# Kernel tuning notes

Hardware: AMD Instinct MI355X
Metric: run time of the kernel (lower is better)

The kernel has to match this reference:

```python
import jax, jax.numpy as jnp
import numpy as np

SOFTCAP = 50.0  # GEMMA2_TANH_SCALE
N_HEADS = 16

def _rope(x, cos, sin):
    # x: [B,S,H,D]; cos/sin: [S,D/2]; interleaved complex pairs as in apply_rotary_emb
    x0 = x[..., 0::2]
    x1 = x[..., 1::2]
    c = cos[None, :, None, :]
    s = sin[None, :, None, :]
    r0 = x0 * c - x1 * s
    r1 = x0 * s + x1 * c
    return jnp.stack([r0, r1], axis=-1).reshape(x.shape)

def setup_inputs() -> dict:
    key = jax.random.key(0)
    ks = jax.random.split(key, 5)
    B, S, DM = 1, 2048, 2048
    hd = DM // N_HEADS
    scale = 1.0 / np.sqrt(DM)
    x = jax.random.normal(ks[0], (B, S, DM), jnp.float32)
    wq = jax.random.normal(ks[1], (DM, DM), jnp.float32) * scale
    wk = jax.random.normal(ks[2], (DM, DM), jnp.float32) * scale
    wv = jax.random.normal(ks[3], (DM, DM), jnp.float32) * scale
    wo = jax.random.normal(ks[4], (DM, DM), jnp.float32) * scale
    # rotary tables, theta=10000 as in llama
    inv_freq = 10000.0 ** (-jnp.arange(0, hd, 2, dtype=jnp.float32) / hd)
    ang = jnp.arange(S, dtype=jnp.float32)[:, None] * inv_freq[None, :]
    return {"x": x, "wq": wq, "wk": wk, "wv": wv, "wo": wo,
            "freqs_cos": jnp.cos(ang), "freqs_sin": jnp.sin(ang)}

def reference(x, wq, wk, wv, wo, freqs_cos, freqs_sin):
    B, S, DM = x.shape
    H = N_HEADS
    hd = DM // H
    q = (x @ wq).reshape(B, S, H, hd)
    k = (x @ wk).reshape(B, S, H, hd)
    v = (x @ wv).reshape(B, S, H, hd)
    q = _rope(q, freqs_cos, freqs_sin)
    k = _rope(k, freqs_cos, freqs_sin)
    # scores [B,H,S,S]
    scores = jnp.einsum('bqhd,bkhd->bhqk', q, k) / jnp.sqrt(jnp.float32(hd))
    scores = SOFTCAP * jnp.tanh(scores / SOFTCAP)  # gemma2 tanh soft-cap
    causal = jnp.tril(jnp.ones((S, S), dtype=bool))
    scores = jnp.where(causal[None, None], scores, -jnp.inf)
    p = jax.nn.softmax(scores, axis=-1)
    o = jnp.einsum('bhqk,bkhd->bqhd', p, v).reshape(B, S, DM)
    return o @ wo
```

## Files before the change

### kernel.cpp

```cpp
#include <hip/hip_runtime.h>
#include <hip/hip_bf16.h>

typedef __attribute__((ext_vector_type(8))) short short8;
typedef __attribute__((ext_vector_type(4))) short short4v;
typedef __attribute__((ext_vector_type(4))) float f32x4;
typedef __attribute__((ext_vector_type(4))) float float4v;

#define S_LEN 2048
#define DMODEL 2048
#define N_HEADS 16
#define HEAD_DIM 128
#define NKT 32

__device__ __forceinline__ float bf2f(__hip_bfloat16 b) { return __bfloat162float(b); }
__device__ __forceinline__ __hip_bfloat16 f2bf(float f) { return __float2bfloat16(f); }
__device__ __forceinline__ short bfs(float f) {
    union { __hip_bfloat16 b; short s; } x; x.b = __float2bfloat16(f); return x.s;
}
__device__ __forceinline__ float sbf(short s) {
    union { short s; __hip_bfloat16 b; } x; x.s = s; return __bfloat162float(x.b);
}

#if __has_builtin(__builtin_amdgcn_global_load_lds)
#define HAVE_ASYNC_LDS 1
#else
#define HAVE_ASYNC_LDS 0
#endif

__device__ __forceinline__ void stage16(const __hip_bfloat16* g, __hip_bfloat16* ldsbase, int lane) {
#if HAVE_ASYNC_LDS
    __builtin_amdgcn_global_load_lds(
        (const __attribute__((address_space(1))) unsigned int*)g,
        (__attribute__((address_space(3))) unsigned int*)ldsbase,
        16, 0, 0);
#else
    *(short8*)((char*)ldsbase + lane * 16) = *(const short8*)g;
#endif
}

__global__ __launch_bounds__(256) void prep(const float* __restrict__ x,
                                            const float* __restrict__ w0,
                                            const float* __restrict__ w1,
                                            const float* __restrict__ w2,
                                            const float* __restrict__ w3,
                                            __hip_bfloat16* __restrict__ xb,
                                            __hip_bfloat16* __restrict__ o0,
                                            __hip_bfloat16* __restrict__ o1,
                                            __hip_bfloat16* __restrict__ o2,
                                            __hip_bfloat16* __restrict__ o3) {
    const int z = blockIdx.z;
    const int tid = threadIdx.x;
    if (z == 4) {
        size_t base = (((size_t)blockIdx.y * 32 + blockIdx.x) * 256 + tid) * 16;
        for (int i = 0; i < 4; ++i) {
            float4v v = *(const float4v*)(x + base + i * 4);
            short4v p;
            p.x = bfs(v.x); p.y = bfs(v.y); p.z = bfs(v.z); p.w = bfs(v.w);
            *(short4v*)((short*)xb + base + i * 4) = p;
        }
        return;
    }
    const float* in = (z == 0) ? w0 : (z == 1) ? w1 : (z == 2) ? w2 : w3;
    __hip_bfloat16* out = (z == 0) ? o0 : (z == 1) ? o1 : (z == 2) ? o2 : o3;
    __shared__ short tile[64][68];
    const int bx = blockIdx.x * 64;
    const int by = blockIdx.y * 64;
    const int c4 = (tid & 15) * 4;
    for (int rr = 0; rr < 4; ++rr) {
        int r = (tid >> 4) + rr * 16;
        float4v v = *(const float4v*)(in + (size_t)(by + r) * DMODEL + bx + c4);
        short4v p;
        p.x = bfs(v.x); p.y = bfs(v.y); p.z = bfs(v.z); p.w = bfs(v.w);
        *(short4v*)&tile[r][c4] = p;
    }
    __syncthreads();
    const int oc = tid >> 2;
    const int s0 = (tid & 3) * 16;
    short8 a, b;
    for (int i = 0; i < 8; ++i) ((short*)&a)[i] = tile[s0 + i][oc];
    for (int i = 0; i < 8; ++i) ((short*)&b)[i] = tile[s0 + 8 + i][oc];
    *(short8*)((short*)out + (size_t)(bx + oc) * DMODEL + by + s0) = a;
    *(short8*)((short*)out + (size_t)(bx + oc) * DMODEL + by + s0 + 8) = b;
}


#define CFENCE asm volatile("" ::: "memory")
#define BARRIER do { CFENCE; __builtin_amdgcn_s_barrier(); CFENCE; } while (0)
#define WAIT_LGKM0 asm volatile("s_waitcnt lgkmcnt(0)" ::: "memory")
#define WAIT_VM(n) asm volatile("s_waitcnt vmcnt(" #n ")" ::: "memory")


#define STAGE_A8(buf, half, kt) do {                                                        \
    const __hip_bfloat16* gpA_ = A + (size_t)(m0 + (half) * 128 + wave * 16 + rsel) * DMODEL \
                                 + (kt) * 64 + gsrc;                                        \
    __hip_bfloat16* lpA_ = (__hip_bfloat16*)(smem + ((buf) * 2 + (half)) * 8192 + wave * 1024); \
    stage16(gpA_, lpA_, lane);                                                              \
    stage16(gpA_ + (size_t)8 * DMODEL, lpA_ + 512, lane);                                   \
} while (0)

#define STAGE_B8(buf, half, kt) do {                                                        \
    const __hip_bfloat16* gpB_ = Bt + (size_t)(n0 + (half) * 128 + wave * 16 + rsel) * DMODEL \
                                 + (kt) * 64 + gsrc;                                        \
    __hip_bfloat16* lpB_ = (__hip_bfloat16*)(smem + 32768 + ((buf) * 2 + (half)) * 8192 + wave * 1024); \
    stage16(gpB_, lpB_, lane);                                                              \
    stage16(gpB_ + (size_t)8 * DMODEL, lpB_ + 512, lane);                                   \
} while (0)

#define LDA4(buf, mb) do {                                                                  \
    const char* ab_ = (const char*)(smem + ((buf) * 2 + wr) * 8192);                        \
    _Pragma("unroll")                                                                       \
    for (int mt_ = 0; mt_ < 4; ++mt_) {                                                     \
        const int rowL_ = ((mb) + mt_) * 16 + lane15;                                       \
        const int r7_ = rowL_ & 7;                                                          \
        af[(mb) + mt_][0] = *(const short8*)(ab_ + rowL_ * 128 + ((quad ^ r7_) * 16));      \
        af[(mb) + mt_][1] = *(const short8*)(ab_ + rowL_ * 128 + (((4 + quad) ^ r7_) * 16));\
    }                                                                                       \
} while (0)

#define LDB2(buf, nb) do {                                                                  \
    const char* bb_ = (const char*)(smem + 32768 + ((buf) * 2 + hb) * 8192);                \
    _Pragma("unroll")                                                                       \
    for (int nt_ = 0; nt_ < 2; ++nt_) {                                                     \
        const int rowL_ = wc1 * 64 + ((nb) + nt_) * 16 + lane15;                            \
        const int r7_ = rowL_ & 7;                                                          \
        bfr[nt_][0] = *(const short8*)(bb_ + rowL_ * 128 + ((quad ^ r7_) * 16));            \
        bfr[nt_][1] = *(const short8*)(bb_ + rowL_ * 128 + (((4 + quad) ^ r7_) * 16));      \
    }                                                                                       \
} while (0)

#define MFMAQ(mb, nb) do {                                                                  \
    _Pragma("unroll")                                                                       \
    for (int mt_ = 0; mt_ < 4; ++mt_) {                                                     \
        _Pragma("unroll")                                                                   \
        for (int nt_ = 0; nt_ < 2; ++nt_) {                                                 \
            acc[(mb) + mt_][(nb) + nt_] = __builtin_amdgcn_mfma_f32_16x16x32_bf16(          \
                af[(mb) + mt_][0], bfr[nt_][0], acc[(mb) + mt_][(nb) + nt_], 0, 0, 0);      \
            acc[(mb) + mt_][(nb) + nt_] = __builtin_amdgcn_mfma_f32_16x16x32_bf16(          \
                af[(mb) + mt_][1], bfr[nt_][1], acc[(mb) + mt_][(nb) + nt_], 0, 0, 0);      \
        }                                                                                   \
    }                                                                                       \
} while (0)

#define GROUP(g, cur, nxt) do {                                                             \
    const int g_ = (g);                                                                     \
    const bool stB_ = (g_ + 1 < NKT);                                                       \
    const bool stA_ = (g_ + 2 < NKT);                                                       \
                                                     \
    LDA4(cur, 0); LDB2(cur, 0);                                                             \
    if (stB_) STAGE_B8(nxt, 0, g_ + 1);                                                     \
    BARRIER; WAIT_LGKM0;                                                                    \
    __builtin_amdgcn_s_setprio(1); MFMAQ(0, 0); __builtin_amdgcn_s_setprio(0);              \
    BARRIER;                                                                                \
                                                                \
    LDA4(cur, 4);                                                                           \
    if (stB_) STAGE_B8(nxt, 1, g_ + 1);                                                     \
    BARRIER; WAIT_LGKM0;                                                                    \
    __builtin_amdgcn_s_setprio(1); MFMAQ(4, 0); __builtin_amdgcn_s_setprio(0);              \
    BARRIER;                                                                                \
                                                                \
    LDB2(cur, 2);                                                                           \
    if (stA_) STAGE_A8(cur, 0, g_ + 2);                                                     \
    BARRIER; WAIT_LGKM0;                                                                    \
    __builtin_amdgcn_s_setprio(1); MFMAQ(0, 2); __builtin_amdgcn_s_setprio(0);              \
    BARRIER;                                                                                \
                                                                \
    if (stA_) STAGE_A8(cur, 1, g_ + 2);                                                     \
    BARRIER;                                                                                \
    __builtin_amdgcn_s_setprio(1); MFMAQ(4, 2); __builtin_amdgcn_s_setprio(0);              \
    if (stA_) { WAIT_VM(4); } else if (stB_) { WAIT_VM(0); }                                \
    BARRIER;                                                                                \
} while (0)

__global__ __launch_bounds__(512, 2) void gemm_qkv_8ph(const __hip_bfloat16* __restrict__ A,
                                                       const __hip_bfloat16* __restrict__ Bq,
                                                       const __hip_bfloat16* __restrict__ Bk,
                                                       const __hip_bfloat16* __restrict__ Bv,
                                                       __hip_bfloat16* __restrict__ Cq,
                                                       __hip_bfloat16* __restrict__ Ck,
                                                       __hip_bfloat16* __restrict__ Cvt,
                                                       const float* __restrict__ fc,
                                                       const float* __restrict__ fs) {
    __shared__ alignas(16) short smem[65536];

    const int tid = threadIdx.x;
    const int wave = tid >> 6;
    const int lane = tid & 63;
    const int lane15 = lane & 15;
    const int quad = lane >> 4;
    const int wr = wave >> 2;
    const int wc = wave & 3;
    const int wc1 = wc & 1;
    const int hb = wc >> 1;
    const int rsel = lane >> 3;
    const int gsrc = ((lane & 7) ^ rsel) * 8;

    const int which = blockIdx.x >> 3;
    const int n0 = (blockIdx.x & 7) * 256;
    const int m0 = blockIdx.y * 256;
    const __hip_bfloat16* Bt = (which == 0) ? Bq : (which == 1) ? Bk : Bv;

    short8 af[8][2];
    short8 bfr[2][2];
    f32x4 acc[8][4];

    STAGE_A8(0, 0, 0);
    STAGE_B8(0, 0, 0);
    STAGE_A8(0, 1, 0);
    STAGE_B8(0, 1, 0);
    STAGE_A8(1, 0, 1);
    STAGE_A8(1, 1, 1);
#pragma unroll
    for (int i = 0; i < 8; ++i)
#pragma unroll
        for (int j = 0; j < 4; ++j)
            acc[i][j] = {0.f, 0.f, 0.f, 0.f};
    WAIT_VM(4);
    BARRIER;

#pragma unroll 1
    for (int g = 0; g < NKT; g += 2) {
        GROUP(g, 0, 1);
        GROUP(g + 1, 1, 0);
    }

    if (which < 2) {
        __hip_bfloat16* C = (which == 0) ? Cq : Ck;
#pragma unroll
        for (int mt = 0; mt < 8; ++mt)
#pragma unroll
            for (int nt = 0; nt < 4; ++nt) {
                int col = n0 + wc * 64 + nt * 16 + lane15;
                int j = (col & 127) >> 1;
                bool odd = col & 1;
#pragma unroll
                for (int i = 0; i < 4; ++i) {
                    int row = m0 + wr * 128 + mt * 16 + quad * 4 + i;
                    float v = acc[mt][nt][i];
                    float p = __shfl_xor(v, 1, 64);
                    float c = fc[row * 64 + j];
                    float sn = fs[row * 64 + j];
                    float r = odd ? (p * sn + v * c) : (v * c - p * sn);
                    C[(size_t)row * DMODEL + col] = f2bf(r);
                }
            }
    } else {
#pragma unroll
        for (int mt = 0; mt < 8; ++mt) {
            int rowbase = m0 + wr * 128 + mt * 16 + quad * 4;
#pragma unroll
            for (int nt = 0; nt < 4; ++nt) {
                int col = n0 + wc * 64 + nt * 16 + lane15;
                short4v pk;
                pk.x = bfs(acc[mt][nt][0]);
                pk.y = bfs(acc[mt][nt][1]);
                pk.z = bfs(acc[mt][nt][2]);
                pk.w = bfs(acc[mt][nt][3]);
                *(short4v*)((short*)Cvt + (size_t)col * S_LEN + rowbase) = pk;
            }
        }
    }
}

__global__ __launch_bounds__(256) void gemm_out(const __hip_bfloat16* __restrict__ A,
                                                const __hip_bfloat16* __restrict__ Bt,
                                                float* __restrict__ C) {
    __shared__ alignas(16) __hip_bfloat16 As[2][128 * 32];
    __shared__ alignas(16) __hip_bfloat16 Bs[2][64 * 32];
    const int tid = threadIdx.x;
    const int wave = tid >> 6;
    const int lane = tid & 63;
    const int lane15 = lane & 15;
    const int quad = lane >> 4;
    const int m0 = blockIdx.y * 128;
    const int n0 = blockIdx.x * 64;
    const int wm = (wave >> 1) * 64;
    const int wn = (wave & 1) * 32;
    f32x4 acc[4][2];
    for (int i = 0; i < 4; ++i)
        for (int j = 0; j < 2; ++j)
            acc[i][j] = {0.f, 0.f, 0.f, 0.f};
    const int rA = lane >> 2;
    const int cA = (lane & 3) * 8;
    for (int k0 = 0; k0 < DMODEL; k0 += 64) {
        __syncthreads();
        for (int h = 0; h < 2; ++h) {
            int kk = k0 + h * 32;
            for (int c = 0; c < 3; ++c) {
                int chunk = wave * 3 + c;
                if (chunk < 8) {
                    int r = chunk * 16 + rA;
                    stage16(A + (size_t)(m0 + r) * DMODEL + kk + cA, As[h] + chunk * 512, lane);
                } else {
                    int r = (chunk - 8) * 16 + rA;
                    stage16(Bt + (size_t)(n0 + r) * DMODEL + kk + cA, Bs[h] + (chunk - 8) * 512, lane);
                }
            }
        }
#if HAVE_ASYNC_LDS
        asm volatile("s_waitcnt vmcnt(0)" ::: "memory");
#endif
        __syncthreads();
        for (int h = 0; h < 2; ++h) {
            short8 af[4], bfr[2];
            for (int mt = 0; mt < 4; ++mt)
                af[mt] = *(const short8*)(As[h] + (wm + mt * 16 + lane15) * 32 + quad * 8);
            for (int nt = 0; nt < 2; ++nt)
                bfr[nt] = *(const short8*)(Bs[h] + (wn + nt * 16 + lane15) * 32 + quad * 8);
            for (int mt = 0; mt < 4; ++mt)
                for (int nt = 0; nt < 2; ++nt)
                    acc[mt][nt] = __builtin_amdgcn_mfma_f32_16x16x32_bf16(af[mt], bfr[nt], acc[mt][nt], 0, 0, 0);
        }
    }
    for (int mt = 0; mt < 4; ++mt)
        for (int nt = 0; nt < 2; ++nt)
            for (int i = 0; i < 4; ++i) {
                int row = m0 + wm + mt * 16 + quad * 4 + i;
                int col = n0 + wn + nt * 16 + lane15;
                C[(size_t)row * DMODEL + col] = acc[mt][nt][i];
            }
}

__global__ __launch_bounds__(256) void flash_attn(const __hip_bfloat16* __restrict__ Q,
                                                  const __hip_bfloat16* __restrict__ Kb,
                                                  const __hip_bfloat16* __restrict__ Vt,
                                                  __hip_bfloat16* __restrict__ O) {
    __shared__ alignas(16) short Ks[32][136];
    __shared__ alignas(16) short Vs[128][40];
    __shared__ alignas(16) short Pl[4][16][40];
    const int tid = threadIdx.x;
    const int wave = tid >> 6;
    const int lane = tid & 63;
    const int lane15 = lane & 15;
    const int quad = lane >> 4;
    const int bx = blockIdx.x;
    const int u = bx & 255;
    const int head = u & 15;
    const int qp = u >> 4;
    const int qb = (bx < 256) ? (31 - qp) : qp;
    const int qbase = qb * 64;
    const int q0w = qbase + wave * 16;
    const int nkt = 2 * qb + 2;
    const float K1 = 0.08838834764831845f * (1.0f / 25.0f);

    const __hip_bfloat16* Qh = Q + (size_t)q0w * DMODEL + head * HEAD_DIM;
    short8 qf[4];
    for (int kk = 0; kk < 4; ++kk)
        qf[kk] = *(const short8*)(Qh + (size_t)lane15 * DMODEL + kk * 32 + quad * 8);

    f32x4 acc[8];
    for (int i = 0; i < 8; ++i) acc[i] = {0.f, 0.f, 0.f, 0.f};
    float lpart[4] = {0.f, 0.f, 0.f, 0.f};

    const int krow = tid >> 3, kcol = (tid & 7) * 16;
    const int vrow = tid >> 1, vcol = (tid & 1) * 16;
    const __hip_bfloat16* Kg = Kb + (size_t)krow * DMODEL + head * HEAD_DIM + kcol;
    const __hip_bfloat16* Vg = Vt + (size_t)(head * HEAD_DIM + vrow) * S_LEN + vcol;

    short8 gk0 = *(const short8*)(Kg);
    short8 gk1 = *(const short8*)(Kg + 8);
    short8 gv0 = *(const short8*)(Vg);
    short8 gv1 = *(const short8*)(Vg + 8);

    for (int kt = 0; kt < nkt; ++kt) {
        const int kb = kt * 32;
        __syncthreads();
        *(short8*)&Ks[krow][kcol] = gk0;
        *(short8*)&Ks[krow][kcol + 8] = gk1;
        *(short8*)&Vs[vrow][vcol] = gv0;
        *(short8*)&Vs[vrow][vcol + 8] = gv1;
        __syncthreads();

        if (kt + 1 < nkt) {
            const __hip_bfloat16* Kg2 = Kg + (size_t)(kb + 32) * DMODEL;
            const __hip_bfloat16* Vg2 = Vg + kb + 32;
            gk0 = *(const short8*)(Kg2);
            gk1 = *(const short8*)(Kg2 + 8);
            gv0 = *(const short8*)(Vg2);
            gv1 = *(const short8*)(Vg2 + 8);
        }

        if (kb <= q0w + 15) {
            f32x4 sc[2];
            sc[0] = {0.f, 0.f, 0.f, 0.f};
            sc[1] = {0.f, 0.f, 0.f, 0.f};
            for (int c = 0; c < 2; ++c)
                for (int kk = 0; kk < 4; ++kk) {
                    short8 kf = *(const short8*)&Ks[c * 16 + lane15][kk * 32 + quad * 8];
                    sc[c] = __builtin_amdgcn_mfma_f32_16x16x32_bf16(qf[kk], kf, sc[c], 0, 0, 0);
                }

            const bool masked = (kb + 31 > q0w);
            const int key0 = kb + lane15;
            const int key1 = kb + 16 + lane15;
            for (int i = 0; i < 4; ++i) {
                float e0 = __expf(sc[0][i] * K1);
                float e1 = __expf(sc[1][i] * K1);
                float c0 = __builtin_fmaf(-100.0f, __builtin_amdgcn_rcpf(e0 + 1.0f), 40.0f);
                float c1 = __builtin_fmaf(-100.0f, __builtin_amdgcn_rcpf(e1 + 1.0f), 40.0f);
                float p0 = __expf(c0);
                float p1 = __expf(c1);
                if (masked) {
                    int q = q0w + quad * 4 + i;
                    if (key0 > q) p0 = 0.f;
                    if (key1 > q) p1 = 0.f;
                }
                short b0 = bfs(p0), b1 = bfs(p1);
                lpart[i] += sbf(b0) + sbf(b1);
                Pl[wave][quad * 4 + i][lane15] = b0;
                Pl[wave][quad * 4 + i][16 + lane15] = b1;
            }
            asm volatile("s_waitcnt lgkmcnt(0)" ::: "memory");
            short8 pf = *(const short8*)&Pl[wave][lane15][quad * 8];
            asm volatile("" ::: "memory");
            for (int nt = 0; nt < 8; ++nt) {
                short8 vf = *(const short8*)&Vs[nt * 16 + lane15][quad * 8];
                acc[nt] = __builtin_amdgcn_mfma_f32_16x16x32_bf16(pf, vf, acc[nt], 0, 0, 0);
            }
        }
    }

    for (int i = 0; i < 4; ++i) {
        float l = lpart[i];
        l += __shfl_xor(l, 1, 64);
        l += __shfl_xor(l, 2, 64);
        l += __shfl_xor(l, 4, 64);
        l += __shfl_xor(l, 8, 64);
        float inv = 1.0f / l;
        int row = q0w + quad * 4 + i;
        for (int nt = 0; nt < 8; ++nt) {
            int col = head * HEAD_DIM + nt * 16 + lane15;
            O[(size_t)row * DMODEL + col] = f2bf(acc[nt][i] * inv);
        }
    }
}

extern "C" void kernel_launch(void* const* d_in, const int* in_sizes, int n_in,
                              void* d_out, int out_size, void* d_ws, size_t ws_size,
                              hipStream_t stream) {
    const float* x  = (const float*)d_in[0];
    const float* wq = (const float*)d_in[1];
    const float* wk = (const float*)d_in[2];
    const float* wv = (const float*)d_in[3];
    const float* wo = (const float*)d_in[4];
    const float* fc = (const float*)d_in[5];
    const float* fs = (const float*)d_in[6];
    float* out = (float*)d_out;

    char* ws = (char*)d_ws;
    const size_t MB8 = (size_t)2048 * 2048 * sizeof(__hip_bfloat16);
    __hip_bfloat16* wq_t = (__hip_bfloat16*)(ws + 0 * MB8);
    __hip_bfloat16* wk_t = (__hip_bfloat16*)(ws + 1 * MB8);
    __hip_bfloat16* wv_t = (__hip_bfloat16*)(ws + 2 * MB8);
    __hip_bfloat16* wo_t = (__hip_bfloat16*)(ws + 3 * MB8);
    __hip_bfloat16* s4   = (__hip_bfloat16*)(ws + 4 * MB8);
    __hip_bfloat16* s5   = (__hip_bfloat16*)(ws + 5 * MB8);
    __hip_bfloat16* s6   = (__hip_bfloat16*)(ws + 6 * MB8);
    __hip_bfloat16* x_bf = (__hip_bfloat16*)d_out;

    prep<<<dim3(32, 32, 5), 256, 0, stream>>>(x, wq, wk, wv, wo, x_bf, wq_t, wk_t, wv_t, wo_t);

    gemm_qkv_8ph<<<dim3(24, 8), 512, 0, stream>>>(x_bf, wq_t, wk_t, wv_t, s4, s5, s6, fc, fs);

    flash_attn<<<512, 256, 0, stream>>>(s4, s5, s6, wq_t);
    gemm_out<<<dim3(32, 16), 256, 0, stream>>>(wq_t, wo_t, out);
}
```

Baseline: 298.2 us.

## Collapse QKV GEMM k-step phases into two barrier-separated halves

The QKV projection GEMM inner step used to run four sub-phases, each with its own LDS fragment load, barrier and MFMA block. It now loads all A and B fragments for the k-tile up front, issues the next B-tile staging, and runs two MFMA halves separated by a single barrier before the A staging. This cuts barriers per group from eight to two and gives the scheduler more independent work to overlap LDS reads with MFMAs. In exchange it holds a larger B fragment array in registers, which may raise VGPR pressure under the 512-thread, 2-block launch bound and risk spills or lower occupancy.

```diff
diff --git a/kernel.cpp b/kernel.cpp
--- a/kernel.cpp
+++ b/kernel.cpp
@@ -106,22 +106,22 @@
     stage16(gpB_ + (size_t)8 * DMODEL, lpB_ + 512, lane);                                   \
 } while (0)
 
-#define LDA4(buf, mb) do {                                                                  \
+#define LDA_ALL(buf) do {                                                                   \
     const char* ab_ = (const char*)(smem + ((buf) * 2 + wr) * 8192);                        \
     _Pragma("unroll")                                                                       \
-    for (int mt_ = 0; mt_ < 4; ++mt_) {                                                     \
-        const int rowL_ = ((mb) + mt_) * 16 + lane15;                                       \
+    for (int mt_ = 0; mt_ < 8; ++mt_) {                                                     \
+        const int rowL_ = mt_ * 16 + lane15;                                                \
         const int r7_ = rowL_ & 7;                                                          \
-        af[(mb) + mt_][0] = *(const short8*)(ab_ + rowL_ * 128 + ((quad ^ r7_) * 16));      \
-        af[(mb) + mt_][1] = *(const short8*)(ab_ + rowL_ * 128 + (((4 + quad) ^ r7_) * 16));\
+        af[mt_][0] = *(const short8*)(ab_ + rowL_ * 128 + ((quad ^ r7_) * 16));             \
+        af[mt_][1] = *(const short8*)(ab_ + rowL_ * 128 + (((4 + quad) ^ r7_) * 16));       \
     }                                                                                       \
 } while (0)
 
-#define LDB2(buf, nb) do {                                                                  \
+#define LDB_ALL(buf) do {                                                                   \
     const char* bb_ = (const char*)(smem + 32768 + ((buf) * 2 + hb) * 8192);                \
     _Pragma("unroll")                                                                       \
-    for (int nt_ = 0; nt_ < 2; ++nt_) {                                                     \
-        const int rowL_ = wc1 * 64 + ((nb) + nt_) * 16 + lane15;                            \
+    for (int nt_ = 0; nt_ < 4; ++nt_) {                                                     \
+        const int rowL_ = wc1 * 64 + nt_ * 16 + lane15;                                     \
         const int r7_ = rowL_ & 7;                                                          \
         bfr[nt_][0] = *(const short8*)(bb_ + rowL_ * 128 + ((quad ^ r7_) * 16));            \
         bfr[nt_][1] = *(const short8*)(bb_ + rowL_ * 128 + (((4 + quad) ^ r7_) * 16));      \
@@ -134,9 +134,9 @@
         _Pragma("unroll")                                                                   \
         for (int nt_ = 0; nt_ < 2; ++nt_) {                                                 \
             acc[(mb) + mt_][(nb) + nt_] = __builtin_amdgcn_mfma_f32_16x16x32_bf16(          \
-                af[(mb) + mt_][0], bfr[nt_][0], acc[(mb) + mt_][(nb) + nt_], 0, 0, 0);      \
+                af[(mb) + mt_][0], bfr[(nb) + nt_][0], acc[(mb) + mt_][(nb) + nt_], 0, 0, 0); \
             acc[(mb) + mt_][(nb) + nt_] = __builtin_amdgcn_mfma_f32_16x16x32_bf16(          \
-                af[(mb) + mt_][1], bfr[nt_][1], acc[(mb) + mt_][(nb) + nt_], 0, 0, 0);      \
+                af[(mb) + mt_][1], bfr[(nb) + nt_][1], acc[(mb) + mt_][(nb) + nt_], 0, 0, 0); \
         }                                                                                   \
     }                                                                                       \
 } while (0)
@@ -145,29 +145,20 @@
     const int g_ = (g);                                                                     \
     const bool stB_ = (g_ + 1 < NKT);                                                       \
     const bool stA_ = (g_ + 2 < NKT);                                                       \
-                                                     \
-    LDA4(cur, 0); LDB2(cur, 0);                                                             \
-    if (stB_) STAGE_B8(nxt, 0, g_ + 1);                                                     \
-    BARRIER; WAIT_LGKM0;                                                                    \
-    __builtin_amdgcn_s_setprio(1); MFMAQ(0, 0); __builtin_amdgcn_s_setprio(0);              \
-    BARRIER;                                                                                \
-                                                                \
-    LDA4(cur, 4);                                                                           \
-    if (stB_) STAGE_B8(nxt, 1, g_ + 1);                                                     \
-    BARRIER; WAIT_LGKM0;                                                                    \
-    __builtin_amdgcn_s_setprio(1); MFMAQ(4, 0); __builtin_amdgcn_s_setprio(0);              \
-    BARRIER;                                                                                \
-                                                                \
-    LDB2(cur, 2);                                                                           \
-    if (stA_) STAGE_A8(cur, 0, g_ + 2);                                                     \
-    BARRIER; WAIT_LGKM0;                                                                    \
-    __builtin_amdgcn_s_setprio(1); MFMAQ(0, 2); __builtin_amdgcn_s_setprio(0);              \
-    BARRIER;                                                                                \
-                                                                \
-    if (stA_) STAGE_A8(cur, 1, g_ + 2);                                                     \
-    BARRIER;                                                                                \
-    __builtin_amdgcn_s_setprio(1); MFMAQ(4, 2); __builtin_amdgcn_s_setprio(0);              \
-    if (stA_) { WAIT_VM(4); } else if (stB_) { WAIT_VM(0); }                                \
+    LDA_ALL(cur);                                                                           \
+    LDB_ALL(cur);                                                                           \
+    if (stB_) { STAGE_B8(nxt, 0, g_ + 1); STAGE_B8(nxt, 1, g_ + 1); }                       \
+    __builtin_amdgcn_s_setprio(1);                                                          \
+    MFMAQ(0, 0); MFMAQ(4, 0);                                                               \
+    __builtin_amdgcn_s_setprio(0);                                                          \
+    WAIT_LGKM0;                             \
+    BARRIER;                     \
+    if (stA_) { STAGE_A8(cur, 0, g_ + 2); STAGE_A8(cur, 1, g_ + 2); }                       \
+    __builtin_amdgcn_s_setprio(1);                                                          \
+    MFMAQ(0, 2); MFMAQ(4, 2);                                                               \
+    __builtin_amdgcn_s_setprio(0);                                                          \
+    if (stA_) { WAIT_VM(4); }               \
+    else if (stB_) { WAIT_VM(0); }          \
     BARRIER;                                                                                \
 } while (0)
 
@@ -200,7 +191,7 @@
     const __hip_bfloat16* Bt = (which == 0) ? Bq : (which == 1) ? Bk : Bv;
 
     short8 af[8][2];
-    short8 bfr[2][2];
+    short8 bfr[4][2];
     f32x4 acc[8][4];
 
     STAGE_A8(0, 0, 0);
```

Measured after the change: 292.5 us. No clear change (-1.9%).
